# Kernel tuning notes

Measured on AMD Instinct MI355X. Metric: run time of the kernel, lower is better.

The kernel has to match this reference:

```python
import jax, jax.numpy as jnp
import numpy as np

B, T, NIN, H1, H2, E, A = 256, 128, 1024, 512, 512, 256, 16
EPS = 1e-5


def setup_inputs() -> dict:
    key = jax.random.key(0)
    ks = jax.random.split(key, 24)
    def lin(k, fan_in, fan_out):
        # weights stored [in, out]; y = x @ W + b (equivalent to torch Linear)
        s = 1.0 / np.sqrt(fan_in)
        kw, kb = jax.random.split(k)
        return (jax.random.uniform(kw, (fan_in, fan_out), jnp.float32, -s, s),
                jax.random.uniform(kb, (fan_out,), jnp.float32, -s, s))
    W1, b1 = lin(ks[0], NIN, H1)
    W2, b2 = lin(ks[1], H1, H2)
    W3, b3 = lin(ks[2], H2, E)
    Wih, bih = lin(ks[3], E, 3 * E)   # GRUCell input weights, gate order [r, z, n]
    Whh, bhh = lin(ks[4], E, 3 * E)   # GRUCell hidden weights
    Whe, bhe = lin(ks[5], E + A, E)   # hidden_encoder
    Wae, bae = lin(ks[6], A, A)       # action_encoder
    return {
        'obs': jax.random.normal(ks[7], (B, T, NIN), jnp.float32),
        'actions': jax.random.normal(ks[8], (B, T, A), jnp.float32),
        'W1': W1, 'b1': b1, 'g1': jnp.ones((H1,), jnp.float32), 'be1': jnp.zeros((H1,), jnp.float32),
        'W2': W2, 'b2': b2, 'g2': jnp.ones((H2,), jnp.float32), 'be2': jnp.zeros((H2,), jnp.float32),
        'W3': W3, 'b3': b3,
        'Wih': Wih, 'bih': bih, 'Whh': Whh, 'bhh': bhh,
        'Whe': Whe, 'bhe': bhe, 'Wae': Wae, 'bae': bae,
    }


def reference(obs, actions, W1, b1, g1, be1, W2, b2, g2, be2, W3, b3,
              Wih, bih, Whh, bhh, Whe, bhe, Wae, bae):
    def bn(x, g, b):  # BatchNorm1d, training mode (batch stats, biased var)
        mu = jnp.mean(x, axis=0)
        var = jnp.mean((x - mu) ** 2, axis=0)
        return g * (x - mu) / jnp.sqrt(var + EPS) + b

    def mlp(x):
        x = jax.nn.elu(bn(x @ W1 + b1, g1, be1))
        x = jax.nn.elu(bn(x @ W2 + b2, g2, be2))
        return x @ W3 + b3

    def gru(x, h):
        gi = x @ Wih + bih
        gh = h @ Whh + bhh
        ir, iz, inn = jnp.split(gi, 3, axis=1)
        hr, hz, hn = jnp.split(gh, 3, axis=1)
        r = jax.nn.sigmoid(ir + hr)
        z = jax.nn.sigmoid(iz + hz)
        n = jnp.tanh(inn + r * hn)
        return (1.0 - z) * n + z * h

    obs_t = jnp.swapaxes(obs, 0, 1)       # [T, B, NIN]
    act_t = jnp.swapaxes(actions, 0, 1)   # [T, B, A]
    h0 = jnp.zeros((obs.shape[0], E), jnp.float32)
    a0 = jnp.zeros((obs.shape[0], A), jnp.float32)

    def step(carry, xs):
        h, a_prev = carry
        o, a = xs
        h = jnp.concatenate([h, a_prev], axis=1) @ Whe + bhe
        a_prev = a @ Wae + bae
        h = gru(mlp(o), h)
        return (h, a_prev), None

    (h, _), _ = jax.lax.scan(step, (h0, a0), (obs_t, act_t))
    return h
```

## Files before the change

kernel.cpp:

```cpp
#include <hip/hip_runtime.h>
#include <math.h>
#include <stdint.h>

#define B_   256
#define T_   128
#define NIN_ 1024
#define H1_  512
#define E_   256
#define A_   16
#define MT_  (B_ * T_)

typedef unsigned short ushort_t;
typedef __attribute__((ext_vector_type(8))) short   short8;
typedef __attribute__((ext_vector_type(8))) __bf16  bf16x8;
typedef __attribute__((ext_vector_type(4))) float   f32x4;

union frag8 { short8 s; bf16x8 b; };

__device__ __forceinline__ ushort_t f2bf(float f) {
  union { float f; unsigned u; } v; v.f = f;
  unsigned r = (v.u + 0x7FFFu + ((v.u >> 16) & 1u)) >> 16;
  return (ushort_t)r;
}

static constexpr size_t OFF_C0    = 0;
static constexpr size_t OFF_OBSB  = 0;
static constexpr size_t OFF_Y     = 134217728;
static constexpr size_t OFF_YG    = 134217728;
static constexpr size_t OFF_XG    = 167772160;
static constexpr size_t OFF_PENCB = 184549376;
static constexpr size_t OFF_XB    = 201326592;
static constexpr size_t OFF_INN   = 201326592;
static constexpr size_t OFF_AE    = 234881024;
static constexpr size_t OFF_W1T   = 236978176;
static constexpr size_t OFF_W2T   = 238026752;
static constexpr size_t OFF_W3T   = 238551040;
static constexpr size_t OFF_WIHT  = 239075328;
static constexpr size_t OFF_WHHT  = 239468544;
static constexpr size_t OFF_WCT   = 240123904;
static constexpr size_t OFF_BSUM  = 241172480;


__global__ __launch_bounds__(256) void cast_obs_k(const float* __restrict__ obs,
                                                  ushort_t* __restrict__ out) {
  int row_in = blockIdx.x;
  int b = row_in / T_, t = row_in - b * T_;
  const float4* s4 = (const float4*)(obs + (size_t)row_in * NIN_);
  float4 v = s4[threadIdx.x];
  ushort_t* d = out + (size_t)(t * B_ + b) * NIN_ + threadIdx.x * 4;
  d[0] = f2bf(v.x); d[1] = f2bf(v.y); d[2] = f2bf(v.z); d[3] = f2bf(v.w);
}

__global__ __launch_bounds__(256) void transpose_cast_k(const float* __restrict__ in,
                                                        ushort_t* __restrict__ out,
                                                        int R, int C) {
  __shared__ float tile[32][33];
  int c0 = blockIdx.x * 32, r0 = blockIdx.y * 32;
  int tx = threadIdx.x & 31, ty = threadIdx.x >> 5;
  for (int i = 0; i < 4; i++) {
    int r = r0 + ty * 4 + i;
    if (r < R && (c0 + tx) < C) tile[ty * 4 + i][tx] = in[(size_t)r * C + c0 + tx];
  }
  __syncthreads();
  for (int i = 0; i < 4; i++) {
    int c = c0 + ty * 4 + i, r = r0 + tx;
    if (c < C && r < R) out[(size_t)c * R + r] = f2bf(tile[tx][ty * 4 + i]);
  }
}

__global__ __launch_bounds__(256) void wct_a_k(const float* __restrict__ Whe,
                                               ushort_t* __restrict__ Wct) {
  int c = blockIdx.x, k = threadIdx.x;
  Wct[(size_t)c * 256 + k] = f2bf(Whe[(size_t)k * 256 + c]);
}

__global__ __launch_bounds__(256) void wct_b_k(const float* __restrict__ Whe,
                                               const float* __restrict__ Whh,
                                               ushort_t* __restrict__ Wct) {
  int c = blockIdx.x;
  int k = threadIdx.x;
  float acc = 0.f;
  for (int j = 0; j < 256; j++)
    acc += Whe[(size_t)k * 256 + j] * Whh[(size_t)j * 768 + c];
  Wct[(size_t)(256 + c) * 256 + k] = f2bf(acc);
}

__global__ void bsum_k(const float* __restrict__ bih, const float* __restrict__ bhh,
                       float* __restrict__ bs) {
  int i = blockIdx.x * 256 + threadIdx.x;
  if (i < 768) bs[i] = bih[i] + bhh[i];
}

__global__ __launch_bounds__(256) void ae_k(const float* __restrict__ actions,
                                            const float* __restrict__ Wae,
                                            const float* __restrict__ bae,
                                            float* __restrict__ AE) {
  int idx = blockIdx.x * 256 + threadIdx.x;
  int m = idx >> 4, k2 = idx & 15;
  int t = m >> 8, b = m & 255;
  const float* arow = actions + ((size_t)b * T_ + t) * A_;
  float acc = bae[k2];
  for (int k = 0; k < 16; k++) acc += arow[k] * Wae[k * 16 + k2];
  AE[(size_t)m * 16 + k2] = acc;
}

__global__ __launch_bounds__(256) void penc_k(const float* __restrict__ AE,
                                              const float* __restrict__ Whe,
                                              const float* __restrict__ bhe,
                                              float* __restrict__ C0,
                                              ushort_t* __restrict__ Pencb) {
  int m = blockIdx.x;
  int j = threadIdx.x;
  __shared__ float a[16];
  if (threadIdx.x < 16)
    a[threadIdx.x] = (m >= B_) ? AE[(size_t)(m - B_) * 16 + threadIdx.x] : 0.f;
  __syncthreads();
  float acc = bhe[j];
  if (m >= B_) {
    for (int k = 0; k < 16; k++) acc += a[k] * Whe[(size_t)(256 + k) * 256 + j];
  }
  C0[(size_t)m * 1024 + j] = acc;
  Pencb[(size_t)m * 256 + j] = f2bf(acc);
}

__global__ __launch_bounds__(512) void bn_elu_k(const float* __restrict__ Y,
                                                const float* __restrict__ g,
                                                const float* __restrict__ be,
                                                ushort_t* __restrict__ Xb) {
  int t = blockIdx.x, f = threadIdx.x;
  const float* base = Y + (size_t)t * B_ * H1_;
  float s = 0.f, ss = 0.f;
  for (int b = 0; b < B_; b++) {
    float v = base[(size_t)b * H1_ + f];
    s += v; ss += v * v;
  }
  float mu  = s * (1.f / B_);
  float var = ss * (1.f / B_) - mu * mu;
  float inv = 1.f / sqrtf(var + 1e-5f);
  float sc = g[f] * inv, sh = be[f] - mu * sc;
  ushort_t* ob = Xb + (size_t)t * B_ * H1_;
  for (int b = 0; b < B_; b++) {
    float v = base[(size_t)b * H1_ + f] * sc + sh;
    float e = v > 0.f ? v : (expf(v) - 1.f);
    ob[(size_t)b * H1_ + f] = f2bf(e);
  }
}

__global__ __launch_bounds__(256) void cast_k(const float* __restrict__ in,
                                              ushort_t* __restrict__ out, long n) {
  long i = (long)blockIdx.x * 256 + threadIdx.x;
  if (i < n) out[i] = f2bf(in[i]);
}

__global__ __launch_bounds__(256) void gemm_bt_k(const ushort_t* __restrict__ A, int lda,
                                                 const ushort_t* __restrict__ Bt, int ldb,
                                                 float* __restrict__ C, int ldc,
                                                 const float* __restrict__ bias,
                                                 int K, int accum) {
  __shared__ __align__(16) ushort_t As[64][40];
  __shared__ __align__(16) ushort_t Bs[64][40];
  int tid = threadIdx.x;
  int wave = tid >> 6, lane = tid & 63;
  int q = lane >> 4, l15 = lane & 15;
  int wr = wave >> 1, wc = wave & 1;
  int m0 = blockIdx.x * 64, n0 = blockIdx.y * 64;
  f32x4 acc[2][2] = {};
  int r = tid >> 2, seg = tid & 3;
  const ushort_t* aSrc = A + (size_t)(m0 + r) * lda + seg * 8;
  const ushort_t* bSrc = Bt + (size_t)(n0 + r) * ldb + seg * 8;
  for (int k0 = 0; k0 < K; k0 += 32) {
    *(short8*)&As[r][seg * 8] = *(const short8*)(aSrc + k0);
    *(short8*)&Bs[r][seg * 8] = *(const short8*)(bSrc + k0);
    __syncthreads();
    frag8 a0, a1, b0, b1;
    a0.s = *(const short8*)&As[wr * 32 + l15][q * 8];
    a1.s = *(const short8*)&As[wr * 32 + 16 + l15][q * 8];
    b0.s = *(const short8*)&Bs[wc * 32 + l15][q * 8];
    b1.s = *(const short8*)&Bs[wc * 32 + 16 + l15][q * 8];
    acc[0][0] = __builtin_amdgcn_mfma_f32_16x16x32_bf16(a0.b, b0.b, acc[0][0], 0, 0, 0);
    acc[0][1] = __builtin_amdgcn_mfma_f32_16x16x32_bf16(a0.b, b1.b, acc[0][1], 0, 0, 0);
    acc[1][0] = __builtin_amdgcn_mfma_f32_16x16x32_bf16(a1.b, b0.b, acc[1][0], 0, 0, 0);
    acc[1][1] = __builtin_amdgcn_mfma_f32_16x16x32_bf16(a1.b, b1.b, acc[1][1], 0, 0, 0);
    __syncthreads();
  }
  for (int at = 0; at < 2; at++)
    for (int bt = 0; bt < 2; bt++) {
      int mb = m0 + wr * 32 + at * 16 + q * 4;
      int n  = n0 + wc * 32 + bt * 16 + l15;
      float bv = bias ? bias[n] : 0.f;
      for (int i = 0; i < 4; i++) {
        size_t idx = (size_t)(mb + i) * ldc + n;
        float v = acc[at][bt][i] + bv;
        if (accum) v += C[idx];
        C[idx] = v;
      }
    }
}

__global__ __launch_bounds__(512, 1) void gru_rows_k(
    const ushort_t* __restrict__ Wct,
    const float* __restrict__ C0,
    const float* __restrict__ INN,
    float* __restrict__ outF) {
  __shared__ __align__(16) ushort_t Wn[256][264];
  __shared__ __align__(16) ushort_t hbuf[2][16][264];
  const int tid = threadIdx.x;
  const int w = tid >> 6, lane = tid & 63;
  const int q = lane >> 4, l15 = lane & 15;
  const int r0 = blockIdx.x * 16;
  const int col0 = w * 32;

  {
    unsigned* hz = (unsigned*)hbuf;
    for (int i = tid; i < 2 * 16 * 264 / 2; i += 512) hz[i] = 0u;
  }
  for (int i = tid; i < 256 * 32; i += 512) {
    int rr = i >> 5, ss = i & 31;
    *(short8*)&Wn[rr][ss * 8] = *(const short8*)(Wct + (size_t)(768 + rr) * 256 + ss * 8);
  }

  frag8 whe_s[2][8];
#pragma unroll
  for (int u = 0; u < 2; u++) {
    const ushort_t* p = Wct + (size_t)(col0 + u * 16 + l15) * 256 + q * 8;
#pragma unroll
    for (int kc = 0; kc < 8; kc++) whe_s[u][kc].s = *(const short8*)(p + kc * 32);
  }
  const ushort_t* wr0 = Wct + (size_t)(256 + col0 + l15) * 256 + q * 8;
  const ushort_t* wr1 = wr0 + (size_t)16 * 256;
  const ushort_t* wz0 = Wct + (size_t)(512 + col0 + l15) * 256 + q * 8;
  const ushort_t* wz1 = wz0 + (size_t)16 * 256;

  __syncthreads();

  for (int t = 0; t < T_; t++) {
    const int cur = t & 1, nxt = cur ^ 1;
    const float* c0t  = C0  + ((size_t)t * B_ + r0) * 1024;
    const float* innt = INN + ((size_t)t * B_ + r0) * 256;

    float c0g[4][2][4], innv[2][4];
#pragma unroll
    for (int u = 0; u < 2; u++) {
      int hc = col0 + u * 16 + l15;
#pragma unroll
      for (int i = 0; i < 4; i++) {
        int row = q * 4 + i;
        const float* rp = c0t + (size_t)row * 1024 + hc;
        c0g[0][u][i] = rp[0];
        c0g[1][u][i] = rp[256];
        c0g[2][u][i] = rp[512];
        c0g[3][u][i] = rp[768];
        innv[u][i] = innt[(size_t)row * 256 + hc];
      }
    }

    f32x4 acc[4][2] = {};
#pragma unroll
    for (int kc = 0; kc < 8; kc++) {
      frag8 a; a.s = *(const short8*)&hbuf[cur][l15][kc * 32 + q * 8];
      frag8 br0_, br1_, bz0_, bz1_, bn0_, bn1_;
      br0_.s = *(const short8*)(wr0 + kc * 32);
      br1_.s = *(const short8*)(wr1 + kc * 32);
      bz0_.s = *(const short8*)(wz0 + kc * 32);
      bz1_.s = *(const short8*)(wz1 + kc * 32);
      bn0_.s = *(const short8*)&Wn[col0 + l15][kc * 32 + q * 8];
      bn1_.s = *(const short8*)&Wn[col0 + 16 + l15][kc * 32 + q * 8];
      acc[0][0] = __builtin_amdgcn_mfma_f32_16x16x32_bf16(a.b, whe_s[0][kc].b, acc[0][0], 0, 0, 0);
      acc[0][1] = __builtin_amdgcn_mfma_f32_16x16x32_bf16(a.b, whe_s[1][kc].b, acc[0][1], 0, 0, 0);
      acc[1][0] = __builtin_amdgcn_mfma_f32_16x16x32_bf16(a.b, br0_.b, acc[1][0], 0, 0, 0);
      acc[1][1] = __builtin_amdgcn_mfma_f32_16x16x32_bf16(a.b, br1_.b, acc[1][1], 0, 0, 0);
      acc[2][0] = __builtin_amdgcn_mfma_f32_16x16x32_bf16(a.b, bz0_.b, acc[2][0], 0, 0, 0);
      acc[2][1] = __builtin_amdgcn_mfma_f32_16x16x32_bf16(a.b, bz1_.b, acc[2][1], 0, 0, 0);
      acc[3][0] = __builtin_amdgcn_mfma_f32_16x16x32_bf16(a.b, bn0_.b, acc[3][0], 0, 0, 0);
      acc[3][1] = __builtin_amdgcn_mfma_f32_16x16x32_bf16(a.b, bn1_.b, acc[3][1], 0, 0, 0);
    }

#pragma unroll
    for (int u = 0; u < 2; u++) {
      int hc = col0 + u * 16 + l15;
#pragma unroll
      for (int i = 0; i < 4; i++) {
        int row = q * 4 + i;
        float henc = acc[0][u][i] + c0g[0][u][i];
        float rp   = acc[1][u][i] + c0g[1][u][i];
        float zp   = acc[2][u][i] + c0g[2][u][i];
        float hn   = acc[3][u][i] + c0g[3][u][i];
        float rg = 1.f / (1.f + expf(-rp));
        float zg = 1.f / (1.f + expf(-zp));
        float ng = tanhf(innv[u][i] + rg * hn);
        float hv = (1.f - zg) * ng + zg * henc;
        if (t < T_ - 1) hbuf[nxt][row][hc] = f2bf(hv);
        else            outF[(size_t)(r0 + row) * 256 + hc] = hv;
      }
    }
    __syncthreads();
  }
}

extern "C" void kernel_launch(void* const* d_in, const int* in_sizes, int n_in,
                              void* d_out, int out_size, void* d_ws, size_t ws_size,
                              hipStream_t stream) {
  const float* obs     = (const float*)d_in[0];
  const float* actions = (const float*)d_in[1];
  const float* W1  = (const float*)d_in[2];
  const float* b1  = (const float*)d_in[3];
  const float* g1  = (const float*)d_in[4];
  const float* be1 = (const float*)d_in[5];
  const float* W2  = (const float*)d_in[6];
  const float* b2  = (const float*)d_in[7];
  const float* g2  = (const float*)d_in[8];
  const float* be2 = (const float*)d_in[9];
  const float* W3  = (const float*)d_in[10];
  const float* b3  = (const float*)d_in[11];
  const float* Wih = (const float*)d_in[12];
  const float* bih = (const float*)d_in[13];
  const float* Whh = (const float*)d_in[14];
  const float* bhh = (const float*)d_in[15];
  const float* Whe = (const float*)d_in[16];
  const float* bhe = (const float*)d_in[17];
  const float* Wae = (const float*)d_in[18];
  const float* bae = (const float*)d_in[19];

  char* ws = (char*)d_ws;
  float*    C0    = (float*)(ws + OFF_C0);
  ushort_t* obsb  = (ushort_t*)(ws + OFF_OBSB);
  float*    Y     = (float*)(ws + OFF_Y);
  float*    Yg    = (float*)(ws + OFF_YG);
  ushort_t* XG    = (ushort_t*)(ws + OFF_XG);
  ushort_t* Pencb = (ushort_t*)(ws + OFF_PENCB);
  ushort_t* Xb    = (ushort_t*)(ws + OFF_XB);
  float*    INN   = (float*)(ws + OFF_INN);
  float*    AE    = (float*)(ws + OFF_AE);
  ushort_t* W1t   = (ushort_t*)(ws + OFF_W1T);
  ushort_t* W2t   = (ushort_t*)(ws + OFF_W2T);
  ushort_t* W3t   = (ushort_t*)(ws + OFF_W3T);
  ushort_t* Wiht  = (ushort_t*)(ws + OFF_WIHT);
  ushort_t* Whht  = (ushort_t*)(ws + OFF_WHHT);
  ushort_t* Wct   = (ushort_t*)(ws + OFF_WCT);
  float*    bsum  = (float*)(ws + OFF_BSUM);
  float*    outF  = (float*)d_out;

  cast_obs_k<<<MT_, 256, 0, stream>>>(obs, obsb);
  transpose_cast_k<<<dim3(16, 32), 256, 0, stream>>>(W1, W1t, 1024, 512);
  transpose_cast_k<<<dim3(16, 16), 256, 0, stream>>>(W2, W2t, 512, 512);
  transpose_cast_k<<<dim3(8, 16),  256, 0, stream>>>(W3, W3t, 512, 256);
  transpose_cast_k<<<dim3(24, 8),  256, 0, stream>>>(Wih, Wiht, 256, 768);
  transpose_cast_k<<<dim3(24, 8),  256, 0, stream>>>(Whh, Whht, 256, 768);
  wct_a_k<<<256, 256, 0, stream>>>(Whe, Wct);
  wct_b_k<<<768, 256, 0, stream>>>(Whe, Whh, Wct);
  bsum_k<<<3, 256, 0, stream>>>(bih, bhh, bsum);
  ae_k<<<MT_ * 16 / 256, 256, 0, stream>>>(actions, Wae, bae, AE);

  gemm_bt_k<<<dim3(512, 8), 256, 0, stream>>>(obsb, 1024, W1t, 1024, Y, 512, b1, 1024, 0);
  bn_elu_k<<<T_, 512, 0, stream>>>(Y, g1, be1, Xb);
  gemm_bt_k<<<dim3(512, 8), 256, 0, stream>>>(Xb, 512, W2t, 512, Y, 512, b2, 512, 0);
  bn_elu_k<<<T_, 512, 0, stream>>>(Y, g2, be2, Xb);
  gemm_bt_k<<<dim3(512, 4), 256, 0, stream>>>(Xb, 512, W3t, 512, Yg, 256, b3, 512, 0);
  cast_k<<<MT_ * 256 / 256, 256, 0, stream>>>(Yg, XG, (long)MT_ * 256);

  penc_k<<<MT_, 256, 0, stream>>>(AE, Whe, bhe, C0, Pencb);
  gemm_bt_k<<<dim3(512, 8), 256, 0, stream>>>(XG, 256, Wiht, 256, C0 + 256, 1024, bsum, 256, 0);
  gemm_bt_k<<<dim3(512, 8), 256, 0, stream>>>(Pencb, 256, Whht, 256, C0 + 256, 1024, nullptr, 256, 1);
  gemm_bt_k<<<dim3(512, 4), 256, 0, stream>>>(Pencb, 256, Whht + 512 * 256, 256, C0 + 768, 1024, bhh + 512, 256, 0);
  gemm_bt_k<<<dim3(512, 4), 256, 0, stream>>>(XG, 256, Wiht + 512 * 256, 256, INN, 256, bih + 512, 256, 0);

  gru_rows_k<<<16, 512, 0, stream>>>(Wct, C0, INN, outF);
}
```

Baseline: 1.325 ms.

## Split GRU recurrence across 16 waves with one column tile each

The sequential GRU kernel now launches 1024 threads per block instead of 512. Each wave handles a single 16-column tile instead of two, so per-wave MFMA chains, register arrays and per-step loads are halved. The aim is to shorten the serial per-timestep critical path of the 128-step recurrence by spreading the work across more waves. In exchange there are more waves taking part in each step's __syncthreads, and register pressure must fit under the 1024-thread launch bound.

```diff
diff --git a/kernel.cpp b/kernel.cpp
--- a/kernel.cpp
+++ b/kernel.cpp
@@ -197,7 +197,7 @@
     }
 }
 
-__global__ __launch_bounds__(512, 1) void gru_rows_k(
+__global__ __launch_bounds__(1024, 4) void gru_rows_k(
     const ushort_t* __restrict__ Wct,
     const float* __restrict__ C0,
     const float* __restrict__ INN,
@@ -208,90 +208,74 @@
   const int w = tid >> 6, lane = tid & 63;
   const int q = lane >> 4, l15 = lane & 15;
   const int r0 = blockIdx.x * 16;
-  const int col0 = w * 32;
+  const int col0 = w * 16;
 
   {
     unsigned* hz = (unsigned*)hbuf;
-    for (int i = tid; i < 2 * 16 * 264 / 2; i += 512) hz[i] = 0u;
-  }
-  for (int i = tid; i < 256 * 32; i += 512) {
+    for (int i = tid; i < 2 * 16 * 264 / 2; i += 1024) hz[i] = 0u;
+  }
+  for (int i = tid; i < 256 * 32; i += 1024) {
     int rr = i >> 5, ss = i & 31;
     *(short8*)&Wn[rr][ss * 8] = *(const short8*)(Wct + (size_t)(768 + rr) * 256 + ss * 8);
   }
 
-  frag8 whe_s[2][8];
+  frag8 whe_s[8];
+  {
+    const ushort_t* p = Wct + (size_t)(col0 + l15) * 256 + q * 8;
 #pragma unroll
-  for (int u = 0; u < 2; u++) {
-    const ushort_t* p = Wct + (size_t)(col0 + u * 16 + l15) * 256 + q * 8;
-#pragma unroll
-    for (int kc = 0; kc < 8; kc++) whe_s[u][kc].s = *(const short8*)(p + kc * 32);
-  }
-  const ushort_t* wr0 = Wct + (size_t)(256 + col0 + l15) * 256 + q * 8;
-  const ushort_t* wr1 = wr0 + (size_t)16 * 256;
-  const ushort_t* wz0 = Wct + (size_t)(512 + col0 + l15) * 256 + q * 8;
-  const ushort_t* wz1 = wz0 + (size_t)16 * 256;
+    for (int kc = 0; kc < 8; kc++) whe_s[kc].s = *(const short8*)(p + kc * 32);
+  }
+  const ushort_t* wr_ = Wct + (size_t)(256 + col0 + l15) * 256 + q * 8;
+  const ushort_t* wz_ = Wct + (size_t)(512 + col0 + l15) * 256 + q * 8;
 
   __syncthreads();
+
+  const int hc = col0 + l15;
 
   for (int t = 0; t < T_; t++) {
     const int cur = t & 1, nxt = cur ^ 1;
     const float* c0t  = C0  + ((size_t)t * B_ + r0) * 1024;
     const float* innt = INN + ((size_t)t * B_ + r0) * 256;
 
-    float c0g[4][2][4], innv[2][4];
+    float c0g[4][4], innv[4];
 #pragma unroll
-    for (int u = 0; u < 2; u++) {
-      int hc = col0 + u * 16 + l15;
-#pragma unroll
-      for (int i = 0; i < 4; i++) {
-        int row = q * 4 + i;
-        const float* rp = c0t + (size_t)row * 1024 + hc;
-        c0g[0][u][i] = rp[0];
-        c0g[1][u][i] = rp[256];
-        c0g[2][u][i] = rp[512];
-        c0g[3][u][i] = rp[768];
-        innv[u][i] = innt[(size_t)row * 256 + hc];
-      }
+    for (int i = 0; i < 4; i++) {
+      int row = q * 4 + i;
+      const float* rp = c0t + (size_t)row * 1024 + hc;
+      c0g[0][i] = rp[0];
+      c0g[1][i] = rp[256];
+      c0g[2][i] = rp[512];
+      c0g[3][i] = rp[768];
+      innv[i] = innt[(size_t)row * 256 + hc];
     }
 
-    f32x4 acc[4][2] = {};
+    f32x4 acc[4] = {};
 #pragma unroll
     for (int kc = 0; kc < 8; kc++) {
       frag8 a; a.s = *(const short8*)&hbuf[cur][l15][kc * 32 + q * 8];
-      frag8 br0_, br1_, bz0_, bz1_, bn0_, bn1_;
-      br0_.s = *(const short8*)(wr0 + kc * 32);
-      br1_.s = *(const short8*)(wr1 + kc * 32);
-      bz0_.s = *(const short8*)(wz0 + kc * 32);
-      bz1_.s = *(const short8*)(wz1 + kc * 32);
-      bn0_.s = *(const short8*)&Wn[col0 + l15][kc * 32 + q * 8];
-      bn1_.s = *(const short8*)&Wn[col0 + 16 + l15][kc * 32 + q * 8];
-      acc[0][0] = __builtin_amdgcn_mfma_f32_16x16x32_bf16(a.b, whe_s[0][kc].b, acc[0][0], 0, 0, 0);
-      acc[0][1] = __builtin_amdgcn_mfma_f32_16x16x32_bf16(a.b, whe_s[1][kc].b, acc[0][1], 0, 0, 0);
-      acc[1][0] = __builtin_amdgcn_mfma_f32_16x16x32_bf16(a.b, br0_.b, acc[1][0], 0, 0, 0);
-      acc[1][1] = __builtin_amdgcn_mfma_f32_16x16x32_bf16(a.b, br1_.b, acc[1][1], 0, 0, 0);
-      acc[2][0] = __builtin_amdgcn_mfma_f32_16x16x32_bf16(a.b, bz0_.b, acc[2][0], 0, 0, 0);
-      acc[2][1] = __builtin_amdgcn_mfma_f32_16x16x32_bf16(a.b, bz1_.b, acc[2][1], 0, 0, 0);
-      acc[3][0] = __builtin_amdgcn_mfma_f32_16x16x32_bf16(a.b, bn0_.b, acc[3][0], 0, 0, 0);
-      acc[3][1] = __builtin_amdgcn_mfma_f32_16x16x32_bf16(a.b, bn1_.b, acc[3][1], 0, 0, 0);
+      frag8 br_, bz_, bn_;
+      br_.s = *(const short8*)(wr_ + kc * 32);
+      bz_.s = *(const short8*)(wz_ + kc * 32);
+      bn_.s = *(const short8*)&Wn[hc][kc * 32 + q * 8];
+      acc[0] = __builtin_amdgcn_mfma_f32_16x16x32_bf16(a.b, whe_s[kc].b, acc[0], 0, 0, 0);
+      acc[1] = __builtin_amdgcn_mfma_f32_16x16x32_bf16(a.b, br_.b, acc[1], 0, 0, 0);
+      acc[2] = __builtin_amdgcn_mfma_f32_16x16x32_bf16(a.b, bz_.b, acc[2], 0, 0, 0);
+      acc[3] = __builtin_amdgcn_mfma_f32_16x16x32_bf16(a.b, bn_.b, acc[3], 0, 0, 0);
     }
 
 #pragma unroll
-    for (int u = 0; u < 2; u++) {
-      int hc = col0 + u * 16 + l15;
-#pragma unroll
-      for (int i = 0; i < 4; i++) {
-        int row = q * 4 + i;
-        float henc = acc[0][u][i] + c0g[0][u][i];
-        float rp   = acc[1][u][i] + c0g[1][u][i];
-        float zp   = acc[2][u][i] + c0g[2][u][i];
-        float hn   = acc[3][u][i] + c0g[3][u][i];
-        float rg = 1.f / (1.f + expf(-rp));
-        float zg = 1.f / (1.f + expf(-zp));
-        float ng = tanhf(innv[u][i] + rg * hn);
-        float hv = (1.f - zg) * ng + zg * henc;
-        if (t < T_ - 1) hbuf[nxt][row][hc] = f2bf(hv);
-        else            outF[(size_t)(r0 + row) * 256 + hc] = hv;
-      }
+    for (int i = 0; i < 4; i++) {
+      int row = q * 4 + i;
+      float henc = acc[0][i] + c0g[0][i];
+      float rp   = acc[1][i] + c0g[1][i];
+      float zp   = acc[2][i] + c0g[2][i];
+      float hn   = acc[3][i] + c0g[3][i];
+      float rg = 1.f / (1.f + expf(-rp));
+      float zg = 1.f / (1.f + expf(-zp));
+      float ng = tanhf(innv[i] + rg * hn);
+      float hv = (1.f - zg) * ng + zg * henc;
+      if (t < T_ - 1) hbuf[nxt][row][hc] = f2bf(hv);
+      else            outF[(size_t)(r0 + row) * 256 + hc] = hv;
     }
     __syncthreads();
   }
@@ -364,5 +348,5 @@
   gemm_bt_k<<<dim3(512, 4), 256, 0, stream>>>(Pencb, 256, Whht + 512 * 256, 256, C0 + 768, 1024, bhh + 512, 256, 0);
   gemm_bt_k<<<dim3(512, 4), 256, 0, stream>>>(XG, 256, Wiht + 512 * 256, 256, INN, 256, bih + 512, 256, 0);
 
-  gru_rows_k<<<16, 512, 0, stream>>>(Wct, C0, INN, outF);
-}
+  gru_rows_k<<<16, 1024, 0, stream>>>(Wct, C0, INN, outF);
+}
```

After: 1.319 ms. Within noise of the previous version (-0.5%).
